# Optimization experiments

Measured on AMD Instinct MI355X. Metric: run time of the kernel, lower is better.

## Reference

```python
import jax, jax.numpy as jnp
import numpy as np

N = 65536          # flattened batch of latent vectors
D = 64             # latent_dim
K = 1024           # codebook_size


def setup_inputs() -> dict:
    key = jax.random.key(0)
    k1, k2 = jax.random.split(key)
    x = jax.random.normal(k1, (N, D), dtype=jnp.float32)
    # codebook init: uniform(-1/K, 1/K) as in the torch module
    W = jax.random.uniform(k2, (K, D), dtype=jnp.float32,
                           minval=-1.0 / K, maxval=1.0 / K)
    return {"x": x, "W": W}


def reference(x, W):
    L2 = jnp.sum(x * x, axis=1, keepdims=True)          # [N, 1]
    C2 = jnp.sum(W * W, axis=1)[None, :]                # [1, K]
    CL = x @ W.T                                        # [N, K]
    distances = L2 - 2.0 * CL + C2
    closest = jnp.argmin(distances, axis=-1)            # [N] int
    # gather nearest codebook vectors (equivalent to one-hot @ W)
    quantized = W[closest]                              # [N, D]
    return quantized, closest
```

## Files before the change

kernel.cpp:

```cpp
#include <hip/hip_runtime.h>
#include <math.h>

#define NROWS 65536
#define DDIM  64
#define KCB   1024

__global__ void vq_c2_kernel(const float* __restrict__ W, float* __restrict__ C2) {
    int j = blockIdx.x * blockDim.x + threadIdx.x;
    if (j >= KCB) return;
    const float* w = W + (size_t)j * DDIM;
    float r[8];
#pragma unroll
    for (int m = 0; m < 8; ++m) r[m] = __fmul_rn(w[m], w[m]);
#pragma unroll
    for (int i = 8; i < 64; i += 8) {
#pragma unroll
        for (int m = 0; m < 8; ++m)
            r[m] = __fadd_rn(r[m], __fmul_rn(w[i + m], w[i + m]));
    }
    float res = __fadd_rn(
        __fadd_rn(__fadd_rn(r[0], r[1]), __fadd_rn(r[2], r[3])),
        __fadd_rn(__fadd_rn(r[4], r[5]), __fadd_rn(r[6], r[7])));
    C2[j] = res;
}

__global__ void __launch_bounds__(256, 4)
vq_main_kernel(const float* __restrict__ x, const float* __restrict__ W,
               const float* __restrict__ C2, int* __restrict__ cls_i,
               float* __restrict__ cls_f) {
    __shared__ float s_bd[4][64];
    __shared__ int   s_bi[4][64];

    const int lane = threadIdx.x & 63;
    const int s    = __builtin_amdgcn_readfirstlane(threadIdx.x >> 6);
    const int row  = blockIdx.x * 64 + lane;

    const float* xr = x + (size_t)row * DDIM;
    float xv[64];
#pragma unroll
    for (int k = 0; k < 64; k += 4) {
        float4 v = *(const float4*)(xr + k);
        xv[k] = v.x; xv[k + 1] = v.y; xv[k + 2] = v.z; xv[k + 3] = v.w;
    }

    float r[8];
#pragma unroll
    for (int m = 0; m < 8; ++m) r[m] = __fmul_rn(xv[m], xv[m]);
#pragma unroll
    for (int i = 8; i < 64; i += 8) {
#pragma unroll
        for (int m = 0; m < 8; ++m)
            r[m] = __fadd_rn(r[m], __fmul_rn(xv[i + m], xv[i + m]));
    }
    const float L2 = __fadd_rn(
        __fadd_rn(__fadd_rn(r[0], r[1]), __fadd_rn(r[2], r[3])),
        __fadd_rn(__fadd_rn(r[4], r[5]), __fadd_rn(r[6], r[7])));

    float best = INFINITY;
    int   bidx = 0;
    const int j0 = s * 256;
    for (int jj = 0; jj < 256; ++jj) {
        const int j = j0 + jj;
        const float* wr = W + (size_t)j * DDIM;
        float acc = 0.0f;
#pragma unroll
        for (int k = 0; k < 64; ++k)
            acc = __builtin_fmaf(xv[k], wr[k], acc);
        const float dist = __fadd_rn(__fsub_rn(L2, __fmul_rn(2.0f, acc)), C2[j]);
        if (dist < best) { best = dist; bidx = j; }
    }

    s_bd[s][lane] = best;
    s_bi[s][lane] = bidx;
    __syncthreads();

    if (s == 0) {
        float b  = s_bd[0][lane];
        int   bi = s_bi[0][lane];
#pragma unroll
        for (int t = 1; t < 4; ++t) {
            const float d = s_bd[t][lane];
            if (d < b) { b = d; bi = s_bi[t][lane]; }
        }
        cls_i[row] = bi;
        cls_f[row] = (float)bi;
    }
}

__global__ void vq_gather_kernel(const float* __restrict__ W,
                                 const int* __restrict__ cls,
                                 float* __restrict__ outq) {
    const int t = blockIdx.x * blockDim.x + threadIdx.x;
    const int i = t >> 4;
    const int q = t & 15;
    const int j = cls[i];
    const float4 v = *(const float4*)(W + (size_t)j * DDIM + q * 4);
    *(float4*)(outq + (size_t)i * DDIM + q * 4) = v;
}

extern "C" void kernel_launch(void* const* d_in, const int* in_sizes, int n_in,
                              void* d_out, int out_size, void* d_ws, size_t ws_size,
                              hipStream_t stream) {
    const float* x = (const float*)d_in[0];
    const float* W = (const float*)d_in[1];

    float* outq = (float*)d_out;
    float* outi = (float*)d_out + (size_t)NROWS * DDIM;

    float* C2  = (float*)d_ws;
    int*   cls = (int*)((char*)d_ws + 4096);

    hipLaunchKernelGGL(vq_c2_kernel, dim3(KCB / 256), dim3(256), 0, stream, W, C2);
    hipLaunchKernelGGL(vq_main_kernel, dim3(NROWS / 64), dim3(256), 0, stream,
                       x, W, C2, cls, outi);
    hipLaunchKernelGGL(vq_gather_kernel, dim3((NROWS * 16) / 256), dim3(256), 0,
                       stream, W, cls, outq);
}
```

Before: 223.9 us.

## Fuse codebook gather into distance kernel and relax launch bounds

```diff
diff --git a/kernel.cpp b/kernel.cpp
--- a/kernel.cpp
+++ b/kernel.cpp
@@ -24,15 +24,15 @@
     C2[j] = res;
 }
 
-__global__ void __launch_bounds__(256, 4)
+__global__ void __launch_bounds__(256, 2)
 vq_main_kernel(const float* __restrict__ x, const float* __restrict__ W,
-               const float* __restrict__ C2, int* __restrict__ cls_i,
-               float* __restrict__ cls_f) {
+               const float* __restrict__ C2, float* __restrict__ outq,
+               float* __restrict__ outi) {
     __shared__ float s_bd[4][64];
     __shared__ int   s_bi[4][64];
 
     const int lane = threadIdx.x & 63;
-    const int s    = __builtin_amdgcn_readfirstlane(threadIdx.x >> 6);
+    const int s    = threadIdx.x >> 6;
     const int row  = blockIdx.x * 64 + lane;
 
     const float* xr = x + (size_t)row * DDIM;
@@ -56,10 +56,18 @@
         __fadd_rn(__fadd_rn(r[0], r[1]), __fadd_rn(r[2], r[3])),
         __fadd_rn(__fadd_rn(r[4], r[5]), __fadd_rn(r[6], r[7])));
 
-    float best = INFINITY;
-    int   bidx = 0;
     const int j0 = s * 256;
-    for (int jj = 0; jj < 256; ++jj) {
+    float best;
+    int   bidx = j0;
+    {
+        const float* wr = W + (size_t)j0 * DDIM;
+        float acc = 0.0f;
+#pragma unroll
+        for (int k = 0; k < 64; ++k)
+            acc = __builtin_fmaf(xv[k], wr[k], acc);
+        best = __fadd_rn(__fsub_rn(L2, __fmul_rn(2.0f, acc)), C2[j0]);
+    }
+    for (int jj = 1; jj < 256; ++jj) {
         const int j = j0 + jj;
         const float* wr = W + (size_t)j * DDIM;
         float acc = 0.0f;
@@ -82,20 +90,22 @@
             const float d = s_bd[t][lane];
             if (d < b) { b = d; bi = s_bi[t][lane]; }
         }
-        cls_i[row] = bi;
-        cls_f[row] = (float)bi;
+        outi[row] = (float)bi;
+        s_bi[0][lane] = bi;
     }
-}
+    __syncthreads();
 
-__global__ void vq_gather_kernel(const float* __restrict__ W,
-                                 const int* __restrict__ cls,
-                                 float* __restrict__ outq) {
-    const int t = blockIdx.x * blockDim.x + threadIdx.x;
-    const int i = t >> 4;
-    const int q = t & 15;
-    const int j = cls[i];
-    const float4 v = *(const float4*)(W + (size_t)j * DDIM + q * 4);
-    *(float4*)(outq + (size_t)i * DDIM + q * 4) = v;
+    {
+        const int t      = threadIdx.x;
+        const int rloc   = t >> 2;
+        const int quart  = t & 3;
+        const int j      = s_bi[0][rloc];
+        const float* src = W + (size_t)j * DDIM + quart * 16;
+        float* dst = outq + ((size_t)blockIdx.x * 64 + rloc) * DDIM + quart * 16;
+#pragma unroll
+        for (int u = 0; u < 4; ++u)
+            *(float4*)(dst + 4 * u) = *(const float4*)(src + 4 * u);
+    }
 }
 
 extern "C" void kernel_launch(void* const* d_in, const int* in_sizes, int n_in,
@@ -107,12 +117,9 @@
     float* outq = (float*)d_out;
     float* outi = (float*)d_out + (size_t)NROWS * DDIM;
 
-    float* C2  = (float*)d_ws;
-    int*   cls = (int*)((char*)d_ws + 4096);
+    float* C2 = (float*)d_ws;
 
     hipLaunchKernelGGL(vq_c2_kernel, dim3(KCB / 256), dim3(256), 0, stream, W, C2);
     hipLaunchKernelGGL(vq_main_kernel, dim3(NROWS / 64), dim3(256), 0, stream,
-                       x, W, C2, cls, outi);
-    hipLaunchKernelGGL(vq_gather_kernel, dim3((NROWS * 16) / 256), dim3(256), 0,
-                       stream, W, cls, outq);
+                       x, W, C2, outq, outi);
 }
```

After: 534.3 us. +138.6%, slower.
